# Kernel tuning notes

Measured on AMD Instinct MI355X. Metric: run time of the kernel, lower is better.

The kernel has to match this reference:

```python
import jax, jax.numpy as jnp
import numpy as np

EMBED_DIM = 1024
NUM_HEADS = 16
HEAD_DIM = EMBED_DIM // NUM_HEADS


def setup_inputs() -> dict:
    key = jax.random.key(0)
    k_x, k_wqkv, k_bqkv, k_wo, k_bo = jax.random.split(key, 5)
    B, T, C = 8, 1024, EMBED_DIM
    s = 1.0 / np.sqrt(C)
    return {
        "x": jax.random.normal(k_x, (B, T, C), dtype=jnp.float32),
        "W_qkv": jax.random.uniform(k_wqkv, (C, 3 * C), minval=-s, maxval=s, dtype=jnp.float32),
        "b_qkv": jax.random.uniform(k_bqkv, (3 * C,), minval=-s, maxval=s, dtype=jnp.float32),
        "W_out": jax.random.uniform(k_wo, (C, C), minval=-s, maxval=s, dtype=jnp.float32),
        "b_out": jax.random.uniform(k_bo, (C,), minval=-s, maxval=s, dtype=jnp.float32),
    }


def reference(x, W_qkv, b_qkv, W_out, b_out):
    B, T, C = x.shape
    H, D = NUM_HEADS, HEAD_DIM
    qkv = x @ W_qkv + b_qkv                      # [B,T,3C]
    q, k, v = jnp.split(qkv, 3, axis=-1)
    q = q.reshape(B, T, H, D).transpose(0, 2, 1, 3)  # [B,H,T,D]
    k = k.reshape(B, T, H, D).transpose(0, 2, 1, 3)
    v = v.reshape(B, T, H, D).transpose(0, 2, 1, 3)
    scores = jnp.einsum("bhqd,bhkd->bhqk", q, k) / np.sqrt(D).astype(np.float32)
    causal = jnp.tril(jnp.ones((T, T), dtype=bool))
    scores = jnp.where(causal[None, None], scores, -jnp.inf)
    attn = jax.nn.softmax(scores, axis=-1)       # dropout is identity in eval
    out = jnp.einsum("bhqk,bhkd->bhqd", attn, v)
    out = out.transpose(0, 2, 1, 3).reshape(B, T, C)
    return out @ W_out + b_out
```

## Files before the change

kernel.cpp:

```cpp
#include <hip/hip_runtime.h>
#include <hip/hip_bf16.h>
#include <cstdint>

using bf16 = __hip_bfloat16;
typedef short short8 __attribute__((ext_vector_type(8)));
typedef float floatx4 __attribute__((ext_vector_type(4)));

#define QSCALE 0.1803368801111601f

__device__ __forceinline__ void async_load16(const bf16* g, bf16* l) {
    __builtin_amdgcn_global_load_lds(
        (const __attribute__((address_space(1))) uint32_t*)g,
        (__attribute__((address_space(3))) uint32_t*)l, 16, 0, 0);
}

__device__ __forceinline__ void bar_lgkm0() {
    asm volatile("s_waitcnt lgkmcnt(0)\ns_barrier" ::: "memory");
}
__device__ __forceinline__ void bar_vm4() {
    asm volatile("s_waitcnt vmcnt(4)\ns_barrier" ::: "memory");
}
__device__ __forceinline__ void bar_vm0() {
    asm volatile("s_waitcnt vmcnt(0)\ns_barrier" ::: "memory");
}

__device__ __forceinline__ uint32_t pack2(float a, float b) {
    union { bf16 h[2]; uint32_t u; } p;
    p.h[0] = __float2bfloat16(a);
    p.h[1] = __float2bfloat16(b);
    return p.u;
}

__global__ __launch_bounds__(256)
void cvt_bf16_kernel(const float* __restrict__ in, bf16* __restrict__ out) {
    const int i = (blockIdx.x * 256 + threadIdx.x) * 4;
    const float4 v = *(const float4*)(in + i);
    bf16 o[4] = {__float2bfloat16(v.x), __float2bfloat16(v.y),
                 __float2bfloat16(v.z), __float2bfloat16(v.w)};
    *(ushort4*)(out + i) = *(ushort4*)o;
}

__global__ __launch_bounds__(256)
void transpose_cvt_kernel(const float* __restrict__ in, bf16* __restrict__ out,
                          int R, int C) {
    __shared__ float tile[32][33];
    const int tx = threadIdx.x & 31, ty = threadIdx.x >> 5;
    const int c0 = blockIdx.x * 32, r0 = blockIdx.y * 32;
    #pragma unroll
    for (int i = 0; i < 32; i += 8)
        tile[ty + i][tx] = in[(size_t)(r0 + ty + i) * C + c0 + tx];
    __syncthreads();
    #pragma unroll
    for (int i = 0; i < 32; i += 8)
        out[(size_t)(c0 + ty + i) * R + r0 + tx] = __float2bfloat16(tile[tx][ty + i]);
}

template <int MODE>
__global__ __launch_bounds__(256, 4)
void gemm_bt_kernel(const bf16* __restrict__ A, const bf16* __restrict__ Bt,
                    const float* __restrict__ bias, int K,
                    bf16* __restrict__ o0, bf16* __restrict__ o1,
                    float* __restrict__ fout) {
    __shared__ bf16 As[2][128 * 32];
    __shared__ bf16 Bs[2][128 * 32];
    const int tid = threadIdx.x;
    const int wave = tid >> 6, lane = tid & 63;
    const int ln = lane & 15, quad = lane >> 4;
    const int wm = wave & 1, wn = wave >> 1;
    const int m0 = blockIdx.y * 128, n0 = blockIdx.x * 128;

    floatx4 acc[4][4] = {};
    const int nkt = K >> 5;

    #pragma unroll
    for (int c = 0; c < 2; ++c) {
        const int e = (c * 256 + tid) * 8;
        async_load16(A + (size_t)(m0 + (e >> 5)) * K + (e & 31),
                     &As[0][(c * 256 + wave * 64) * 8]);
    }
    #pragma unroll
    for (int c = 0; c < 2; ++c) {
        const int e = (c * 256 + tid) * 8;
        async_load16(Bt + (size_t)(n0 + (e >> 5)) * K + (e & 31),
                     &Bs[0][(c * 256 + wave * 64) * 8]);
    }

    for (int kt = 0; kt < nkt; ++kt) {
        const int cur = kt & 1;
        bar_lgkm0();
        if (kt + 1 < nkt) {
            const int k0 = (kt + 1) << 5;
            #pragma unroll
            for (int c = 0; c < 2; ++c) {
                const int e = (c * 256 + tid) * 8;
                async_load16(A + (size_t)(m0 + (e >> 5)) * K + k0 + (e & 31),
                             &As[cur ^ 1][(c * 256 + wave * 64) * 8]);
            }
            #pragma unroll
            for (int c = 0; c < 2; ++c) {
                const int e = (c * 256 + tid) * 8;
                async_load16(Bt + (size_t)(n0 + (e >> 5)) * K + k0 + (e & 31),
                             &Bs[cur ^ 1][(c * 256 + wave * 64) * 8]);
            }
            bar_vm4();
        } else {
            bar_vm0();
        }

        short8 af[4], bfr[4];
        #pragma unroll
        for (int i = 0; i < 4; ++i) {
            af[i]  = *(const short8*)&As[cur][(wm * 64 + i * 16 + ln) * 32 + quad * 8];
            bfr[i] = *(const short8*)&Bs[cur][(wn * 64 + i * 16 + ln) * 32 + quad * 8];
        }
        #pragma unroll
        for (int mi = 0; mi < 4; ++mi)
            #pragma unroll
            for (int ni = 0; ni < 4; ++ni)
                acc[mi][ni] = __builtin_amdgcn_mfma_f32_16x16x32_bf16(
                    af[mi], bfr[ni], acc[mi][ni], 0, 0, 0);
    }

    if (MODE == 0) {
        #pragma unroll
        for (int mi = 0; mi < 4; ++mi) {
            const int ch0 = m0 + wm * 64 + mi * 16 + quad * 4;
            const int which = ch0 >> 10;
            const int h = (ch0 & 1023) >> 6, d0 = ch0 & 63;
            const float4 bv = *(const float4*)&bias[ch0];
            bf16* dst = which ? o1 : o0;
            #pragma unroll
            for (int ni = 0; ni < 4; ++ni) {
                const int tok = n0 + wn * 64 + ni * 16 + ln;
                const int bb = tok >> 10, t = tok & 1023;
                float v0 = acc[mi][ni][0] + bv.x;
                float v1 = acc[mi][ni][1] + bv.y;
                float v2 = acc[mi][ni][2] + bv.z;
                float v3 = acc[mi][ni][3] + bv.w;
                if (which == 0) { v0 *= QSCALE; v1 *= QSCALE; v2 *= QSCALE; v3 *= QSCALE; }
                const int dd = (((d0 >> 3) ^ (t & 7)) << 3) | (d0 & 7);
                uint2 w2 = { pack2(v0, v1), pack2(v2, v3) };
                *(uint2*)&dst[((size_t)(bb * 16 + h) * 1024 + t) * 64 + dd] = w2;
            }
        }
    } else if (MODE == 2) {
        #pragma unroll
        for (int ni = 0; ni < 4; ++ni) {
            const int col = n0 + wn * 64 + ni * 16 + ln;
            const int h = col >> 6, d = col & 63;
            const float bv = bias[col];
            #pragma unroll
            for (int mi = 0; mi < 4; ++mi) {
                const int rowb = m0 + wm * 64 + mi * 16 + quad * 4;
                const int bb = rowb >> 10, t = rowb & 1023;
                const int tl = t & 63;
                const int tt = (t & ~63) + ((((tl >> 3) ^ (d & 7)) << 3) | (tl & 7));
                uint2 w2 = { pack2(acc[mi][ni][0] + bv, acc[mi][ni][1] + bv),
                             pack2(acc[mi][ni][2] + bv, acc[mi][ni][3] + bv) };
                *(uint2*)&o0[((size_t)(bb * 16 + h) * 64 + d) * 1024 + tt] = w2;
            }
        }
    } else {
        #pragma unroll
        for (int mi = 0; mi < 4; ++mi) {
            const int ch0 = m0 + wm * 64 + mi * 16 + quad * 4;
            const float4 bv = *(const float4*)&bias[ch0];
            #pragma unroll
            for (int ni = 0; ni < 4; ++ni) {
                const int tok = n0 + wn * 64 + ni * 16 + ln;
                float4 o = { acc[mi][ni][0] + bv.x, acc[mi][ni][1] + bv.y,
                             acc[mi][ni][2] + bv.z, acc[mi][ni][3] + bv.w };
                *(float4*)&fout[(size_t)tok * 1024 + ch0] = o;
            }
        }
    }
}

__global__ __launch_bounds__(256, 3)
void attn_kernel(const bf16* __restrict__ Q, const bf16* __restrict__ K,
                 const bf16* __restrict__ Vt, bf16* __restrict__ O) {
    constexpr int T = 1024;
    __shared__ bf16 QPs[128 * 64];
    __shared__ bf16 Ks[2][64 * 64];
    __shared__ bf16 Vts[2][64 * 64];

    const int bh = blockIdx.y;
    const int tid = threadIdx.x;
    const int wave = tid >> 6, lane = tid & 63;
    const int ln = lane & 15, quad = lane >> 4;

    const bf16* Kg = K + (size_t)bh * T * 64;
    const bf16* Vg = Vt + (size_t)bh * 64 * T;
    const int b = bh >> 4, h = bh & 15;

    #pragma unroll
    for (int phase = 0; phase < 2; ++phase) {
        const int jt = phase ? 7 - blockIdx.x : blockIdx.x;
        const int q0 = jt * 128;
        const int nkt = 2 * jt + 2;

        bar_lgkm0();

        const bf16* Qg = Q + (size_t)bh * T * 64 + (size_t)q0 * 64;
        #pragma unroll
        for (int c = 0; c < 4; ++c)
            async_load16(Qg + (size_t)(c * 256 + tid) * 8,
                         &QPs[(c * 256 + wave * 64) * 8]);
        #pragma unroll
        for (int c = 0; c < 2; ++c)
            async_load16(Kg + (size_t)(c * 256 + tid) * 8,
                         &Ks[0][(c * 256 + wave * 64) * 8]);
        #pragma unroll
        for (int c = 0; c < 2; ++c) {
            const int e = (c * 256 + tid) * 8;
            async_load16(Vg + (size_t)(e >> 6) * T + (e & 63),
                         &Vts[0][(c * 256 + wave * 64) * 8]);
        }
        bar_vm0();

        short8 bq[2][2];
        #pragma unroll
        for (int qj = 0; qj < 2; ++qj)
            #pragma unroll
            for (int ks = 0; ks < 2; ++ks) {
                const int row = wave * 32 + qj * 16 + ln;
                const int ch = (ks * 4 + quad) ^ (row & 7);
                bq[qj][ks] = *(const short8*)&QPs[row * 64 + ch * 8];
            }

        floatx4 oacc[4][2] = {};
        float rm[2] = {-1e30f, -1e30f}, rl[2] = {0.f, 0.f};
        const int qbw = q0 + wave * 32;

        for (int kt = 0; kt < nkt; ++kt) {
            const int cur = kt & 1;
            bar_lgkm0();
            if (kt + 1 < nkt) {
                const int nxt = cur ^ 1;
                #pragma unroll
                for (int c = 0; c < 2; ++c)
                    async_load16(Kg + (size_t)(kt + 1) * 4096 + (size_t)(c * 256 + tid) * 8,
                                 &Ks[nxt][(c * 256 + wave * 64) * 8]);
                #pragma unroll
                for (int c = 0; c < 2; ++c) {
                    const int e = (c * 256 + tid) * 8;
                    async_load16(Vg + (size_t)(e >> 6) * T + (kt + 1) * 64 + (e & 63),
                                 &Vts[nxt][(c * 256 + wave * 64) * 8]);
                }
                bar_vm4();
            } else {
                bar_vm0();
            }

            const int k0 = kt * 64;
            if (k0 > qbw + 31) continue;
            const bool tail = (k0 + 63 > qbw);

            floatx4 sacc[4][2] = {};
            #pragma unroll
            for (int nj = 0; nj < 4; ++nj) {
                if (tail && k0 + nj * 16 > qbw + 31) continue;
                short8 ak[2];
                #pragma unroll
                for (int ks = 0; ks < 2; ++ks) {
                    const int row = nj * 16 + ln;
                    const int ch = (ks * 4 + quad) ^ (row & 7);
                    ak[ks] = *(const short8*)&Ks[cur][row * 64 + ch * 8];
                }
                #pragma unroll
                for (int qj = 0; qj < 2; ++qj) {
                    if (tail && k0 + nj * 16 > qbw + qj * 16 + 15) continue;
                    #pragma unroll
                    for (int ks = 0; ks < 2; ++ks)
                        sacc[nj][qj] = __builtin_amdgcn_mfma_f32_16x16x32_bf16(
                            ak[ks], bq[qj][ks], sacc[nj][qj], 0, 0, 0);
                }
            }

            if (tail) {
                #pragma unroll
                for (int nj = 0; nj < 4; ++nj)
                    #pragma unroll
                    for (int qj = 0; qj < 2; ++qj) {
                        const int qq = qbw + qj * 16 + ln;
                        #pragma unroll
                        for (int r = 0; r < 4; ++r) {
                            const int kk = k0 + nj * 16 + quad * 4 + r;
                            if (kk > qq) sacc[nj][qj][r] = -1e30f;
                        }
                    }
            }

            #pragma unroll
            for (int qj = 0; qj < 2; ++qj) {
                float mx = sacc[0][qj][0];
                #pragma unroll
                for (int nj = 0; nj < 4; ++nj)
                    #pragma unroll
                    for (int r = 0; r < 4; ++r) mx = fmaxf(mx, sacc[nj][qj][r]);
                mx = fmaxf(mx, __shfl_xor(mx, 16, 64));
                mx = fmaxf(mx, __shfl_xor(mx, 32, 64));
                const float mn = fmaxf(rm[qj], mx);
                const float alpha = exp2f(rm[qj] - mn);
                rm[qj] = mn;
                rl[qj] *= alpha;
                #pragma unroll
                for (int dt = 0; dt < 4; ++dt) oacc[dt][qj] *= alpha;
                float rs = 0.f;
                const int qrow = wave * 32 + qj * 16 + ln;
                #pragma unroll
                for (int nj = 0; nj < 4; ++nj) {
                    float p[4];
                    #pragma unroll
                    for (int r = 0; r < 4; ++r) {
                        p[r] = exp2f(sacc[nj][qj][r] - mn);
                        rs += p[r];
                    }
                    const int kcol = nj * 16 + quad * 4;
                    const int ch = (kcol >> 3) ^ (qrow & 7);
                    uint2 w2 = { pack2(p[0], p[1]), pack2(p[2], p[3]) };
                    *(uint2*)&QPs[qrow * 64 + ch * 8 + (kcol & 7)] = w2;
                }
                rl[qj] += rs;
            }

            #pragma unroll
            for (int ks4 = 0; ks4 < 2; ++ks4) {
                short8 bp[2];
                #pragma unroll
                for (int qj = 0; qj < 2; ++qj) {
                    const int qrow = wave * 32 + qj * 16 + ln;
                    const int ch = (ks4 * 4 + quad) ^ (qrow & 7);
                    bp[qj] = *(const short8*)&QPs[qrow * 64 + ch * 8];
                }
                #pragma unroll
                for (int dt = 0; dt < 4; ++dt) {
                    const int row = dt * 16 + ln;
                    const int ch = (ks4 * 4 + quad) ^ (row & 7);
                    const short8 av = *(const short8*)&Vts[cur][row * 64 + ch * 8];
                    #pragma unroll
                    for (int qj = 0; qj < 2; ++qj)
                        oacc[dt][qj] = __builtin_amdgcn_mfma_f32_16x16x32_bf16(
                            av, bp[qj], oacc[dt][qj], 0, 0, 0);
                }
            }
        }

        #pragma unroll
        for (int qj = 0; qj < 2; ++qj) {
            float l = rl[qj];
            l += __shfl_xor(l, 16, 64);
            l += __shfl_xor(l, 32, 64);
            const float inv = 1.0f / l;
            const int t = q0 + wave * 32 + qj * 16 + ln;
            const size_t rowb = ((size_t)b * 1024 + t) * 1024 + h * 64;
            #pragma unroll
            for (int dt = 0; dt < 4; ++dt) {
                uint2 w2 = { pack2(oacc[dt][qj][0] * inv, oacc[dt][qj][1] * inv),
                             pack2(oacc[dt][qj][2] * inv, oacc[dt][qj][3] * inv) };
                *(uint2*)&O[rowb + dt * 16 + quad * 4] = w2;
            }
        }
    }
}

extern "C" void kernel_launch(void* const* d_in, const int* in_sizes, int n_in,
                              void* d_out, int out_size, void* d_ws, size_t ws_size,
                              hipStream_t stream) {
    const float* x     = (const float*)d_in[0];
    const float* W_qkv = (const float*)d_in[1];
    const float* b_qkv = (const float*)d_in[2];
    const float* W_out = (const float*)d_in[3];
    const float* b_out = (const float*)d_in[4];
    float* out = (float*)d_out;

    char* ws = (char*)d_ws;
    const size_t MB = 1u << 20;
    bf16* x_bf   = (bf16*)(ws + 0);
    bf16* wqkv_t = (bf16*)(ws + 16 * MB);
    bf16* wout_t = (bf16*)(ws + 22 * MB);
    bf16* q_ws   = (bf16*)(ws + 24 * MB);
    bf16* k_ws   = (bf16*)(ws + 40 * MB);
    bf16* vt_ws  = (bf16*)(ws + 56 * MB);
    bf16* ao_ws  = (bf16*)(ws + 72 * MB);

    cvt_bf16_kernel<<<8192, 256, 0, stream>>>(x, x_bf);
    transpose_cvt_kernel<<<dim3(96, 32), 256, 0, stream>>>(W_qkv, wqkv_t, 1024, 3072);
    transpose_cvt_kernel<<<dim3(32, 32), 256, 0, stream>>>(W_out, wout_t, 1024, 1024);

    gemm_bt_kernel<0><<<dim3(64, 16), 256, 0, stream>>>(
        wqkv_t, x_bf, b_qkv, 1024, q_ws, k_ws, nullptr);
    gemm_bt_kernel<2><<<dim3(8, 64), 256, 0, stream>>>(
        x_bf, wqkv_t + (size_t)2048 * 1024, b_qkv + 2048, 1024, vt_ws, nullptr, nullptr);

    attn_kernel<<<dim3(4, 128), 256, 0, stream>>>(q_ws, k_ws, vt_ws, ao_ws);

    gemm_bt_kernel<1><<<dim3(64, 8), 256, 0, stream>>>(
        wout_t, ao_ws, b_out, 1024, nullptr, nullptr, out);
}
```

Before: 255.2 us.

## Shrink attention query tile to 64 rows, one 16-row slice per wave

```diff
diff --git a/kernel.cpp b/kernel.cpp
--- a/kernel.cpp
+++ b/kernel.cpp
@@ -176,11 +176,11 @@
     }
 }
 
-__global__ __launch_bounds__(256, 3)
+__global__ __launch_bounds__(256, 4)
 void attn_kernel(const bf16* __restrict__ Q, const bf16* __restrict__ K,
                  const bf16* __restrict__ Vt, bf16* __restrict__ O) {
     constexpr int T = 1024;
-    __shared__ bf16 QPs[128 * 64];
+    __shared__ bf16 QPs[64 * 64];
     __shared__ bf16 Ks[2][64 * 64];
     __shared__ bf16 Vts[2][64 * 64];
 
@@ -195,15 +195,15 @@
 
     #pragma unroll
     for (int phase = 0; phase < 2; ++phase) {
-        const int jt = phase ? 7 - blockIdx.x : blockIdx.x;
-        const int q0 = jt * 128;
-        const int nkt = 2 * jt + 2;
+        const int jt = phase ? 15 - blockIdx.x : blockIdx.x;
+        const int q0 = jt * 64;
+        const int nkt = jt + 1;
 
         bar_lgkm0();
 
         const bf16* Qg = Q + (size_t)bh * T * 64 + (size_t)q0 * 64;
         #pragma unroll
-        for (int c = 0; c < 4; ++c)
+        for (int c = 0; c < 2; ++c)
             async_load16(Qg + (size_t)(c * 256 + tid) * 8,
                          &QPs[(c * 256 + wave * 64) * 8]);
         #pragma unroll
@@ -218,19 +218,17 @@
         }
         bar_vm0();
 
-        short8 bq[2][2];
-        #pragma unroll
-        for (int qj = 0; qj < 2; ++qj)
-            #pragma unroll
-            for (int ks = 0; ks < 2; ++ks) {
-                const int row = wave * 32 + qj * 16 + ln;
-                const int ch = (ks * 4 + quad) ^ (row & 7);
-                bq[qj][ks] = *(const short8*)&QPs[row * 64 + ch * 8];
-            }
-
-        floatx4 oacc[4][2] = {};
-        float rm[2] = {-1e30f, -1e30f}, rl[2] = {0.f, 0.f};
-        const int qbw = q0 + wave * 32;
+        short8 bq[2];
+        #pragma unroll
+        for (int ks = 0; ks < 2; ++ks) {
+            const int row = wave * 16 + ln;
+            const int ch = (ks * 4 + quad) ^ (row & 7);
+            bq[ks] = *(const short8*)&QPs[row * 64 + ch * 8];
+        }
+
+        floatx4 oacc[4] = {};
+        float rm = -1e30f, rl = 0.f;
+        const int qbw = q0 + wave * 16;
 
         for (int kt = 0; kt < nkt; ++kt) {
             const int cur = kt & 1;
@@ -253,67 +251,56 @@
             }
 
             const int k0 = kt * 64;
-            if (k0 > qbw + 31) continue;
+            if (k0 > qbw + 15) continue;
             const bool tail = (k0 + 63 > qbw);
 
-            floatx4 sacc[4][2] = {};
+            floatx4 sacc[4] = {};
             #pragma unroll
             for (int nj = 0; nj < 4; ++nj) {
-                if (tail && k0 + nj * 16 > qbw + 31) continue;
-                short8 ak[2];
+                if (tail && k0 + nj * 16 > qbw + 15) continue;
                 #pragma unroll
                 for (int ks = 0; ks < 2; ++ks) {
                     const int row = nj * 16 + ln;
                     const int ch = (ks * 4 + quad) ^ (row & 7);
-                    ak[ks] = *(const short8*)&Ks[cur][row * 64 + ch * 8];
+                    const short8 ak = *(const short8*)&Ks[cur][row * 64 + ch * 8];
+                    sacc[nj] = __builtin_amdgcn_mfma_f32_16x16x32_bf16(
+                        ak, bq[ks], sacc[nj], 0, 0, 0);
                 }
-                #pragma unroll
-                for (int qj = 0; qj < 2; ++qj) {
-                    if (tail && k0 + nj * 16 > qbw + qj * 16 + 15) continue;
-                    #pragma unroll
-                    for (int ks = 0; ks < 2; ++ks)
-                        sacc[nj][qj] = __builtin_amdgcn_mfma_f32_16x16x32_bf16(
-                            ak[ks], bq[qj][ks], sacc[nj][qj], 0, 0, 0);
-                }
             }
 
             if (tail) {
+                const int qq = qbw + ln;
                 #pragma unroll
                 for (int nj = 0; nj < 4; ++nj)
                     #pragma unroll
-                    for (int qj = 0; qj < 2; ++qj) {
-                        const int qq = qbw + qj * 16 + ln;
-                        #pragma unroll
-                        for (int r = 0; r < 4; ++r) {
-                            const int kk = k0 + nj * 16 + quad * 4 + r;
-                            if (kk > qq) sacc[nj][qj][r] = -1e30f;
-                        }
+                    for (int r = 0; r < 4; ++r) {
+                        const int kk = k0 + nj * 16 + quad * 4 + r;
+                        if (kk > qq) sacc[nj][r] = -1e30f;
                     }
             }
 
-            #pragma unroll
-            for (int qj = 0; qj < 2; ++qj) {
-                float mx = sacc[0][qj][0];
+            {
+                float mx = sacc[0][0];
                 #pragma unroll
                 for (int nj = 0; nj < 4; ++nj)
                     #pragma unroll
-                    for (int r = 0; r < 4; ++r) mx = fmaxf(mx, sacc[nj][qj][r]);
+                    for (int r = 0; r < 4; ++r) mx = fmaxf(mx, sacc[nj][r]);
                 mx = fmaxf(mx, __shfl_xor(mx, 16, 64));
                 mx = fmaxf(mx, __shfl_xor(mx, 32, 64));
-                const float mn = fmaxf(rm[qj], mx);
-                const float alpha = exp2f(rm[qj] - mn);
-                rm[qj] = mn;
-                rl[qj] *= alpha;
-                #pragma unroll
-                for (int dt = 0; dt < 4; ++dt) oacc[dt][qj] *= alpha;
+                const float mn = fmaxf(rm, mx);
+                const float alpha = exp2f(rm - mn);
+                rm = mn;
+                rl *= alpha;
+                #pragma unroll
+                for (int dt = 0; dt < 4; ++dt) oacc[dt] *= alpha;
                 float rs = 0.f;
-                const int qrow = wave * 32 + qj * 16 + ln;
+                const int qrow = wave * 16 + ln;
                 #pragma unroll
                 for (int nj = 0; nj < 4; ++nj) {
                     float p[4];
                     #pragma unroll
                     for (int r = 0; r < 4; ++r) {
-                        p[r] = exp2f(sacc[nj][qj][r] - mn);
+                        p[r] = exp2f(sacc[nj][r] - mn);
                         rs += p[r];
                     }
                     const int kcol = nj * 16 + quad * 4;
@@ -321,43 +308,36 @@
                     uint2 w2 = { pack2(p[0], p[1]), pack2(p[2], p[3]) };
                     *(uint2*)&QPs[qrow * 64 + ch * 8 + (kcol & 7)] = w2;
                 }
-                rl[qj] += rs;
+                rl += rs;
             }
 
             #pragma unroll
             for (int ks4 = 0; ks4 < 2; ++ks4) {
-                short8 bp[2];
-                #pragma unroll
-                for (int qj = 0; qj < 2; ++qj) {
-                    const int qrow = wave * 32 + qj * 16 + ln;
-                    const int ch = (ks4 * 4 + quad) ^ (qrow & 7);
-                    bp[qj] = *(const short8*)&QPs[qrow * 64 + ch * 8];
-                }
+                const int qrow = wave * 16 + ln;
+                const int chp = (ks4 * 4 + quad) ^ (qrow & 7);
+                const short8 bp = *(const short8*)&QPs[qrow * 64 + chp * 8];
                 #pragma unroll
                 for (int dt = 0; dt < 4; ++dt) {
                     const int row = dt * 16 + ln;
                     const int ch = (ks4 * 4 + quad) ^ (row & 7);
                     const short8 av = *(const short8*)&Vts[cur][row * 64 + ch * 8];
-                    #pragma unroll
-                    for (int qj = 0; qj < 2; ++qj)
-                        oacc[dt][qj] = __builtin_amdgcn_mfma_f32_16x16x32_bf16(
-                            av, bp[qj], oacc[dt][qj], 0, 0, 0);
+                    oacc[dt] = __builtin_amdgcn_mfma_f32_16x16x32_bf16(
+                        av, bp, oacc[dt], 0, 0, 0);
                 }
             }
         }
 
-        #pragma unroll
-        for (int qj = 0; qj < 2; ++qj) {
-            float l = rl[qj];
+        {
+            float l = rl;
             l += __shfl_xor(l, 16, 64);
             l += __shfl_xor(l, 32, 64);
             const float inv = 1.0f / l;
-            const int t = q0 + wave * 32 + qj * 16 + ln;
+            const int t = q0 + wave * 16 + ln;
             const size_t rowb = ((size_t)b * 1024 + t) * 1024 + h * 64;
             #pragma unroll
             for (int dt = 0; dt < 4; ++dt) {
-                uint2 w2 = { pack2(oacc[dt][qj][0] * inv, oacc[dt][qj][1] * inv),
-                             pack2(oacc[dt][qj][2] * inv, oacc[dt][qj][3] * inv) };
+                uint2 w2 = { pack2(oacc[dt][0] * inv, oacc[dt][1] * inv),
+                             pack2(oacc[dt][2] * inv, oacc[dt][3] * inv) };
                 *(uint2*)&O[rowb + dt * 16 + quad * 4] = w2;
             }
         }
@@ -393,7 +373,7 @@
     gemm_bt_kernel<2><<<dim3(8, 64), 256, 0, stream>>>(
         x_bf, wqkv_t + (size_t)2048 * 1024, b_qkv + 2048, 1024, vt_ws, nullptr, nullptr);
 
-    attn_kernel<<<dim3(4, 128), 256, 0, stream>>>(q_ws, k_ws, vt_ws, ao_ws);
+    attn_kernel<<<dim3(8, 128), 256, 0, stream>>>(q_ws, k_ws, vt_ws, ao_ws);
 
     gemm_bt_kernel<1><<<dim3(64, 8), 256, 0, stream>>>(
         wout_t, ao_ws, b_out, 1024, nullptr, nullptr, out);
```

After: 255.8 us. About the same (+0.2%).
